# Performance work log

Measured on AMD Instinct MI355X. Metric: run time of the kernel, lower is better.

## Reference

```python
import jax, jax.numpy as jnp
import numpy as np

N = 100000   # nodes
C = 128      # in_channels
K = 32       # n_super_nodes
B = 64       # graphs (num segments)


def setup_inputs() -> dict:
    key = jax.random.key(0)
    k_x, k_b, k_w1, k_b1, k_w2, k_b2 = jax.random.split(key, 6)
    x = jax.random.normal(k_x, (N, C), dtype=jnp.float32)
    batch = jnp.sort(jax.random.randint(k_b, (N,), 0, B))
    # assign_mlp params: Linear(C,C) -> ReLU -> Linear(C,K); stored as [in,out]
    W1 = jax.random.normal(k_w1, (C, C), dtype=jnp.float32) / np.sqrt(C)
    b1 = jax.random.normal(k_b1, (C,), dtype=jnp.float32) * 0.01
    W2 = jax.random.normal(k_w2, (C, K), dtype=jnp.float32) / np.sqrt(C)
    b2 = jax.random.normal(k_b2, (K,), dtype=jnp.float32) * 0.01
    return {"x": x, "batch": batch, "W1": W1, "b1": b1, "W2": W2, "b2": b2}


def reference(x, batch, W1, b1, W2, b2):
    # assignment logits: MLP over node features
    h = jax.nn.relu(x @ W1 + b1)          # [N, C]
    s = jax.nn.softmax(h @ W2 + b2, axis=-1)  # [N, K]
    # outer product per node, then scatter-sum by graph id
    x_expanded = x[:, None, :] * s[:, :, None]  # [N, K, C]
    out = jax.ops.segment_sum(x_expanded, batch, num_segments=B)  # [B, K, C]
    return (out, s)
```

## Files before the change

### kernel.cpp

```cpp
#include <hip/hip_runtime.h>
#include <hip/hip_bf16.h>

#define NN 100000
#define CC 128
#define KK 32
#define BB 64
#define PS 16

typedef __bf16 bf16x8 __attribute__((ext_vector_type(8)));
typedef float  f32x4  __attribute__((ext_vector_type(4)));

__device__ __forceinline__ unsigned short f2bf(float v) {
    union { float f; unsigned u; } a; a.f = v;
    unsigned r = a.u + 0x7FFF + ((a.u >> 16) & 1);
    return (unsigned short)(r >> 16);
}
__device__ __forceinline__ float bf2f(unsigned short h) {
    union { unsigned u; float f; } a; a.u = ((unsigned)h) << 16;
    return a.f;
}
__device__ __forceinline__ void unpack_hilo(uint4 a, uint4 b,
                                            bf16x8& hi8, bf16x8& lo8) {
    union { uint4 v[2]; unsigned short s[16]; } U;
    U.v[0] = a; U.v[1] = b;
    union { unsigned short s[8]; bf16x8 v; } H, L;
    #pragma unroll
    for (int j = 0; j < 8; ++j) { H.s[j] = U.s[2 * j]; L.s[j] = U.s[2 * j + 1]; }
    hi8 = H.v; lo8 = L.v;
}

__global__ __launch_bounds__(256) void hp_prep(const int* __restrict__ batch,
                                               const float* __restrict__ W1,
                                               const float* __restrict__ W2,
                                               int* __restrict__ bounds,
                                               unsigned short* __restrict__ w1f,
                                               unsigned short* __restrict__ w2f) {
    if (blockIdx.x == 0 && threadIdx.x <= BB) {
        const int b = threadIdx.x;
        int lo = 0, hi = NN;
        while (lo < hi) {
            const int mid = (lo + hi) >> 1;
            if (batch[mid] < b) lo = mid + 1; else hi = mid;
        }
        bounds[b] = lo;
    }
    const int t = blockIdx.x * 256 + threadIdx.x;
    for (int idx = t; idx < 16384; idx += 2048) {
        const int j    = idx & 7;
        const int lane = (idx >> 3) & 63;
        const int nt   = (idx >> 9) & 7;
        const int kt   = idx >> 12;
        const int k = kt * 32 + (lane >> 4) * 8 + j;
        const int n = nt * 16 + (lane & 15);
        const float w = W1[k * CC + n];
        const unsigned short h = f2bf(w);
        w1f[idx]         = h;
        w1f[16384 + idx] = f2bf(w - bf2f(h));
    }
    for (int idx = t; idx < 4096; idx += 2048) {
        const int j    = idx & 7;
        const int lane = (idx >> 3) & 63;
        const int nt   = (idx >> 9) & 1;
        const int kt   = idx >> 10;
        const int k = kt * 32 + (lane >> 4) * 8 + j;
        const int n = nt * 16 + (lane & 15);
        const float w = W2[k * KK + n];
        const unsigned short h = f2bf(w);
        w2f[idx]        = h;
        w2f[4096 + idx] = f2bf(w - bf2f(h));
    }
}

__global__ __launch_bounds__(256, 6) void hp_mlp(
    const float* __restrict__ x,
    const unsigned short* __restrict__ w1f,
    const unsigned short* __restrict__ w2f,
    const float* __restrict__ b1,
    const float* __restrict__ b2,
    float* __restrict__ s_out,
    unsigned short* __restrict__ xb,
    unsigned short* __restrict__ sb)
{
    __shared__ __align__(16) char uni[16896];
    __shared__ float lgT[32][36];
    __shared__ float redm[4][32];
    __shared__ float reds[4][32];

    unsigned short* xa   = (unsigned short*)uni;
    unsigned int*   hs16 = (unsigned int*)uni;

    const int t    = threadIdx.x;
    const int wave = __builtin_amdgcn_readfirstlane(t >> 6);
    const int lane = t & 63;
    const int base = blockIdx.x * 32;

    #pragma unroll
    for (int mt = 0; mt < 2; ++mt) {
        const int q  = mt * 4 + wave;
        const int n  = base + mt * 16 + (lane & 15);
        const int ck = wave * 32 + (lane >> 4) * 8;
        const float4 va = *(const float4*)(x + (size_t)n * CC + ck);
        const float4 vb = *(const float4*)(x + (size_t)n * CC + ck + 4);
        const float v[8] = {va.x, va.y, va.z, va.w, vb.x, vb.y, vb.z, vb.w};
        unsigned short hi[8], lo[8];
        #pragma unroll
        for (int j = 0; j < 8; ++j) {
            hi[j] = f2bf(v[j]);
            lo[j] = f2bf(v[j] - bf2f(hi[j]));
        }
        unsigned short* d0 = xa + (q * 64 + lane) * 8;
        unsigned short* d1 = d0 + 4096;
        *(ushort4*)(d0)     = make_ushort4(hi[0], hi[1], hi[2], hi[3]);
        *(ushort4*)(d0 + 4) = make_ushort4(hi[4], hi[5], hi[6], hi[7]);
        *(ushort4*)(d1)     = make_ushort4(lo[0], lo[1], lo[2], lo[3]);
        *(ushort4*)(d1 + 4) = make_ushort4(lo[4], lo[5], lo[6], lo[7]);
    }

    #pragma unroll
    for (int cc = 0; cc < 2; ++cc) {
        const int ct = wave * 2 + cc;
        const int c  = ct * 16 + (lane & 15);
        const int nb = base + (lane >> 4) * 8;
        unsigned short hb[8];
        #pragma unroll
        for (int j = 0; j < 8; ++j)
            hb[j] = f2bf(x[(size_t)(nb + j) * CC + c]);
        unsigned short* dp = xb + ((size_t)(blockIdx.x * 8 + ct) * 64 + lane) * 8;
        *(ushort4*)(dp)     = make_ushort4(hb[0], hb[1], hb[2], hb[3]);
        *(ushort4*)(dp + 4) = make_ushort4(hb[4], hb[5], hb[6], hb[7]);
    }
    __syncthreads();

    f32x4 acc[2][2];
    #pragma unroll
    for (int mt = 0; mt < 2; ++mt)
        #pragma unroll
        for (int nl = 0; nl < 2; ++nl)
            acc[mt][nl] = (f32x4){0.f, 0.f, 0.f, 0.f};

    #pragma unroll
    for (int kt = 0; kt < 4; ++kt) {
        bf16x8 ah[2], al[2];
        #pragma unroll
        for (int mt = 0; mt < 2; ++mt) {
            ah[mt] = *(const bf16x8*)(xa + ((mt * 4 + kt) * 64 + lane) * 8);
            al[mt] = *(const bf16x8*)(xa + 4096 + ((mt * 4 + kt) * 64 + lane) * 8);
        }
        #pragma unroll
        for (int nl = 0; nl < 2; ++nl) {
            const int nt = 2 * wave + nl;
            const bf16x8 wh = *(const bf16x8*)(w1f + ((kt * 8 + nt) * 64 + lane) * 8);
            const bf16x8 wl = *(const bf16x8*)(w1f + 16384 + ((kt * 8 + nt) * 64 + lane) * 8);
            #pragma unroll
            for (int mt = 0; mt < 2; ++mt) {
                acc[mt][nl] = __builtin_amdgcn_mfma_f32_16x16x32_bf16(ah[mt], wh, acc[mt][nl], 0, 0, 0);
                acc[mt][nl] = __builtin_amdgcn_mfma_f32_16x16x32_bf16(al[mt], wh, acc[mt][nl], 0, 0, 0);
                acc[mt][nl] = __builtin_amdgcn_mfma_f32_16x16x32_bf16(ah[mt], wl, acc[mt][nl], 0, 0, 0);
            }
        }
    }
    __syncthreads();

    #pragma unroll
    for (int nl = 0; nl < 2; ++nl) {
        const int c = (2 * wave + nl) * 16 + (lane & 15);
        const float bv = b1[c];
        #pragma unroll
        for (int mt = 0; mt < 2; ++mt)
            #pragma unroll
            for (int r = 0; r < 4; ++r) {
                const int node = mt * 16 + (lane >> 4) * 4 + r;
                const float h = fmaxf(acc[mt][nl][r] + bv, 0.f);
                const unsigned short hi = f2bf(h);
                const unsigned short lo = f2bf(h - bf2f(hi));
                hs16[node * 132 + c] = (unsigned)hi | ((unsigned)lo << 16);
            }
    }
    __syncthreads();

    {
        const int mt2 = wave & 1, nt2 = wave >> 1;
        f32x4 dacc = (f32x4){0.f, 0.f, 0.f, 0.f};
        #pragma unroll
        for (int kt = 0; kt < 4; ++kt) {
            const unsigned* hp = hs16 + (mt2 * 16 + (lane & 15)) * 132
                                      + kt * 32 + (lane >> 4) * 8;
            const uint4 u0 = *(const uint4*)hp;
            const uint4 u1 = *(const uint4*)(hp + 4);
            bf16x8 ah, al;
            unpack_hilo(u0, u1, ah, al);
            const bf16x8 wh = *(const bf16x8*)(w2f + ((kt * 2 + nt2) * 64 + lane) * 8);
            const bf16x8 wl = *(const bf16x8*)(w2f + 4096 + ((kt * 2 + nt2) * 64 + lane) * 8);
            dacc = __builtin_amdgcn_mfma_f32_16x16x32_bf16(ah, wh, dacc, 0, 0, 0);
            dacc = __builtin_amdgcn_mfma_f32_16x16x32_bf16(al, wh, dacc, 0, 0, 0);
            dacc = __builtin_amdgcn_mfma_f32_16x16x32_bf16(ah, wl, dacc, 0, 0, 0);
        }
        const int kcol = nt2 * 16 + (lane & 15);
        #pragma unroll
        for (int r = 0; r < 4; ++r) {
            const int node = mt2 * 16 + (lane >> 4) * 4 + r;
            lgT[node][kcol] = dacc[r];
        }
    }
    __syncthreads();

    const int node = lane & 31;
    const int koff = ((lane >> 5) << 4) + wave * 4;
    const float4 bv2 = *(const float4*)(b2 + koff);
    const float4 lv  = *(const float4*)&lgT[node][koff];
    float lg[4] = {lv.x + bv2.x, lv.y + bv2.y, lv.z + bv2.z, lv.w + bv2.w};

    float m = fmaxf(fmaxf(lg[0], lg[1]), fmaxf(lg[2], lg[3]));
    m = fmaxf(m, __shfl_xor(m, 32));
    if (lane < 32) redm[wave][lane] = m;
    __syncthreads();
    const float M = fmaxf(fmaxf(redm[0][node], redm[1][node]),
                          fmaxf(redm[2][node], redm[3][node]));
    const float e0 = __expf(lg[0] - M);
    const float e1 = __expf(lg[1] - M);
    const float e2 = __expf(lg[2] - M);
    const float e3 = __expf(lg[3] - M);
    float sp = (e0 + e1) + (e2 + e3);
    sp += __shfl_xor(sp, 32);
    if (lane < 32) reds[wave][lane] = sp;
    __syncthreads();
    const float S = (reds[0][node] + reds[1][node]) + (reds[2][node] + reds[3][node]);
    const float inv = 1.f / S;
    const float4 s4 = make_float4(e0 * inv, e1 * inv, e2 * inv, e3 * inv);
    *(float4*)(s_out + (size_t)(base + node) * KK + koff) = s4;
    *(float4*)&lgT[node][koff] = s4;
    __syncthreads();

    if (wave < 2) {
        const int k  = wave * 16 + (lane & 15);
        const int r0 = (lane >> 4) * 8;
        unsigned short v[8];
        #pragma unroll
        for (int j = 0; j < 8; ++j)
            v[j] = f2bf(lgT[r0 + j][k]);
        unsigned short* dp = sb + ((size_t)(blockIdx.x * 2 + wave) * 64 + lane) * 8;
        *(ushort4*)(dp)     = make_ushort4(v[0], v[1], v[2], v[3]);
        *(ushort4*)(dp + 4) = make_ushort4(v[4], v[5], v[6], v[7]);
    }
}

__global__ __launch_bounds__(256) void hp_pool(
    const unsigned short* __restrict__ xb,
    const unsigned short* __restrict__ sb,
    const int* __restrict__ bounds,
    float* __restrict__ part)
{
    const int b = blockIdx.x / PS;
    const int p = blockIdx.x - b * PS;
    const int wave = __builtin_amdgcn_readfirstlane(threadIdx.x >> 6);
    const int lane = threadIdx.x & 63;

    const int gs = bounds[b], ge = bounds[b + 1];
    const int c0g = gs >> 5;
    const int cnt = ((ge + 31) >> 5) - c0g;
    const int ch0 = c0g + (cnt * p) / PS;
    const int ch1 = c0g + (cnt * (p + 1)) / PS;

    const int mt    = wave & 1;
    const int chalf = wave >> 1;
    const int nrow  = (lane >> 4) * 8;

    f32x4 acc[4];
    #pragma unroll
    for (int i = 0; i < 4; ++i) acc[i] = (f32x4){0.f, 0.f, 0.f, 0.f};

    for (int ch = ch0; ch < ch1; ++ch) {
        union { ushort4 u[2]; unsigned short s[8]; bf16x8 v; } A;
        const unsigned short* ap = sb + ((size_t)(ch * 2 + mt) * 64 + lane) * 8;
        A.u[0] = *(const ushort4*)ap;
        A.u[1] = *(const ushort4*)(ap + 4);
        const int nb = ch * 32 + nrow;
        #pragma unroll
        for (int j = 0; j < 8; ++j)
            if (nb + j < gs || nb + j >= ge) A.s[j] = 0;
        #pragma unroll
        for (int i = 0; i < 4; ++i) {
            const int ct = chalf * 4 + i;
            const bf16x8 Bv = *(const bf16x8*)(xb + ((size_t)(ch * 8 + ct) * 64 + lane) * 8);
            acc[i] = __builtin_amdgcn_mfma_f32_16x16x32_bf16(A.v, Bv, acc[i], 0, 0, 0);
        }
    }

    float* op = part + (size_t)blockIdx.x * KK * CC;
    #pragma unroll
    for (int i = 0; i < 4; ++i) {
        const int c = (chalf * 4 + i) * 16 + (lane & 15);
        #pragma unroll
        for (int r = 0; r < 4; ++r) {
            const int k = mt * 16 + (lane >> 4) * 4 + r;
            op[k * CC + c] = acc[i][r];
        }
    }
}

__global__ __launch_bounds__(256) void hp_reduce(const float* __restrict__ part,
                                                 float* __restrict__ out) {
    const int i = (blockIdx.x * 256 + threadIdx.x) * 4;
    if (i < BB * KK * CC) {
        const int b = i >> 12;
        const int j = i & 4095;
        const float* pp = part + (size_t)b * PS * 4096 + j;
        float4 r = make_float4(0.f, 0.f, 0.f, 0.f);
        #pragma unroll 4
        for (int q = 0; q < PS; ++q) {
            const float4 v = *(const float4*)(pp + (size_t)q * 4096);
            r.x += v.x; r.y += v.y; r.z += v.z; r.w += v.w;
        }
        *(float4*)(out + i) = r;
    }
}

extern "C" void kernel_launch(void* const* d_in, const int* in_sizes, int n_in,
                              void* d_out, int out_size, void* d_ws, size_t ws_size,
                              hipStream_t stream) {
    const float* x     = (const float*)d_in[0];
    const int*   batch = (const int*)d_in[1];
    const float* W1    = (const float*)d_in[2];
    const float* b1    = (const float*)d_in[3];
    const float* W2    = (const float*)d_in[4];
    const float* b2    = (const float*)d_in[5];

    float* out = (float*)d_out;
    float* s   = out + (size_t)BB * KK * CC;

    char* ws = (char*)d_ws;
    int*            bounds = (int*)ws;
    unsigned short* w1f    = (unsigned short*)(ws + 1024);
    unsigned short* w2f    = (unsigned short*)(ws + 66560);
    unsigned short* xb     = (unsigned short*)(ws + 82944);
    unsigned short* sb     = (unsigned short*)(ws + 82944 + 25600000);
    float*          part   = (float*)(ws + 82944 + 25600000 + 6400000);

    hp_prep<<<8, 256, 0, stream>>>(batch, W1, W2, bounds, w1f, w2f);
    hp_mlp<<<NN / 32, 256, 0, stream>>>(x, w1f, w2f, b1, b2, s, xb, sb);
    hp_pool<<<BB * PS, 256, 0, stream>>>(xb, sb, bounds, part);
    hp_reduce<<<BB * KK * CC / (256 * 4), 256, 0, stream>>>(part, out);
}
```

Before: 133.4 us.

## Replace partial-sum reduce kernel with float atomics and fold output zeroing into prep

Removes the hp_reduce launch and the partial buffer. hp_pool now adds its per-split results straight into the output with hardware float atomics, and hp_prep (grown to 64 blocks) zeroes the output and does the weight conversion without loops. The change also switches bf16 conversion to the native cast, uses v_perm for hi/lo unpacking, and widens stores to uint4. The aim is to save one kernel launch and the round trip of partial sums through memory, in exchange for atomic contention (16 writers per element) and a nondeterministic summation order.

Result: slower. 139.1 us (+4.3%).

```diff
diff --git a/kernel.cpp b/kernel.cpp
--- a/kernel.cpp
+++ b/kernel.cpp
@@ -11,9 +11,9 @@
 typedef float  f32x4  __attribute__((ext_vector_type(4)));
 
 __device__ __forceinline__ unsigned short f2bf(float v) {
-    union { float f; unsigned u; } a; a.f = v;
-    unsigned r = a.u + 0x7FFF + ((a.u >> 16) & 1);
-    return (unsigned short)(r >> 16);
+    union { __bf16 h; unsigned short s; } u;
+    u.h = (__bf16)v;
+    return u.s;
 }
 __device__ __forceinline__ float bf2f(unsigned short h) {
     union { unsigned u; float f; } a; a.u = ((unsigned)h) << 16;
@@ -21,12 +21,24 @@
 }
 __device__ __forceinline__ void unpack_hilo(uint4 a, uint4 b,
                                             bf16x8& hi8, bf16x8& lo8) {
-    union { uint4 v[2]; unsigned short s[16]; } U;
-    U.v[0] = a; U.v[1] = b;
-    union { unsigned short s[8]; bf16x8 v; } H, L;
-    #pragma unroll
-    for (int j = 0; j < 8; ++j) { H.s[j] = U.s[2 * j]; L.s[j] = U.s[2 * j + 1]; }
+    union { unsigned u[4]; bf16x8 v; } H, L;
+    H.u[0] = __builtin_amdgcn_perm(a.y, a.x, 0x05040100u);
+    H.u[1] = __builtin_amdgcn_perm(a.w, a.z, 0x05040100u);
+    H.u[2] = __builtin_amdgcn_perm(b.y, b.x, 0x05040100u);
+    H.u[3] = __builtin_amdgcn_perm(b.w, b.z, 0x05040100u);
+    L.u[0] = __builtin_amdgcn_perm(a.y, a.x, 0x07060302u);
+    L.u[1] = __builtin_amdgcn_perm(a.w, a.z, 0x07060302u);
+    L.u[2] = __builtin_amdgcn_perm(b.y, b.x, 0x07060302u);
+    L.u[3] = __builtin_amdgcn_perm(b.w, b.z, 0x07060302u);
     hi8 = H.v; lo8 = L.v;
+}
+
+__device__ __forceinline__ void atomAddF(float* p, float v) {
+#if defined(__gfx950__) || defined(__gfx942__) || defined(__gfx90a__)
+    unsafeAtomicAdd(p, v);
+#else
+    atomicAdd(p, v);
+#endif
 }
 
 __global__ __launch_bounds__(256) void hp_prep(const int* __restrict__ batch,
@@ -34,7 +46,8 @@
                                                const float* __restrict__ W2,
                                                int* __restrict__ bounds,
                                                unsigned short* __restrict__ w1f,
-                                               unsigned short* __restrict__ w2f) {
+                                               unsigned short* __restrict__ w2f,
+                                               float* __restrict__ out_zero) {
     if (blockIdx.x == 0 && threadIdx.x <= BB) {
         const int b = threadIdx.x;
         int lo = 0, hi = NN;
@@ -45,7 +58,8 @@
         bounds[b] = lo;
     }
     const int t = blockIdx.x * 256 + threadIdx.x;
-    for (int idx = t; idx < 16384; idx += 2048) {
+    {
+        const int idx  = t;
         const int j    = idx & 7;
         const int lane = (idx >> 3) & 63;
         const int nt   = (idx >> 9) & 7;
@@ -57,7 +71,8 @@
         w1f[idx]         = h;
         w1f[16384 + idx] = f2bf(w - bf2f(h));
     }
-    for (int idx = t; idx < 4096; idx += 2048) {
+    if (t < 4096) {
+        const int idx  = t;
         const int j    = idx & 7;
         const int lane = (idx >> 3) & 63;
         const int nt   = (idx >> 9) & 1;
@@ -69,6 +84,10 @@
         w2f[idx]        = h;
         w2f[4096 + idx] = f2bf(w - bf2f(h));
     }
+    const float4 z = make_float4(0.f, 0.f, 0.f, 0.f);
+    #pragma unroll
+    for (int i = t; i < BB * KK * CC / 4; i += 16384)
+        *(float4*)(out_zero + (size_t)i * 4) = z;
 }
 
 __global__ __launch_bounds__(256, 6) void hp_mlp(
@@ -102,18 +121,15 @@
         const float4 va = *(const float4*)(x + (size_t)n * CC + ck);
         const float4 vb = *(const float4*)(x + (size_t)n * CC + ck + 4);
         const float v[8] = {va.x, va.y, va.z, va.w, vb.x, vb.y, vb.z, vb.w};
-        unsigned short hi[8], lo[8];
+        union { unsigned short s[8]; uint4 u; } H, L;
         #pragma unroll
         for (int j = 0; j < 8; ++j) {
-            hi[j] = f2bf(v[j]);
-            lo[j] = f2bf(v[j] - bf2f(hi[j]));
+            H.s[j] = f2bf(v[j]);
+            L.s[j] = f2bf(v[j] - bf2f(H.s[j]));
         }
         unsigned short* d0 = xa + (q * 64 + lane) * 8;
-        unsigned short* d1 = d0 + 4096;
-        *(ushort4*)(d0)     = make_ushort4(hi[0], hi[1], hi[2], hi[3]);
-        *(ushort4*)(d0 + 4) = make_ushort4(hi[4], hi[5], hi[6], hi[7]);
-        *(ushort4*)(d1)     = make_ushort4(lo[0], lo[1], lo[2], lo[3]);
-        *(ushort4*)(d1 + 4) = make_ushort4(lo[4], lo[5], lo[6], lo[7]);
+        *(uint4*)(d0)        = H.u;
+        *(uint4*)(d0 + 4096) = L.u;
     }
 
     #pragma unroll
@@ -121,13 +137,12 @@
         const int ct = wave * 2 + cc;
         const int c  = ct * 16 + (lane & 15);
         const int nb = base + (lane >> 4) * 8;
-        unsigned short hb[8];
+        union { unsigned short s[8]; uint4 u; } Hb;
         #pragma unroll
         for (int j = 0; j < 8; ++j)
-            hb[j] = f2bf(x[(size_t)(nb + j) * CC + c]);
+            Hb.s[j] = f2bf(x[(size_t)(nb + j) * CC + c]);
         unsigned short* dp = xb + ((size_t)(blockIdx.x * 8 + ct) * 64 + lane) * 8;
-        *(ushort4*)(dp)     = make_ushort4(hb[0], hb[1], hb[2], hb[3]);
-        *(ushort4*)(dp + 4) = make_ushort4(hb[4], hb[5], hb[6], hb[7]);
+        *(uint4*)dp = Hb.u;
     }
     __syncthreads();
 
@@ -234,13 +249,12 @@
     if (wave < 2) {
         const int k  = wave * 16 + (lane & 15);
         const int r0 = (lane >> 4) * 8;
-        unsigned short v[8];
+        union { unsigned short s[8]; uint4 u; } V;
         #pragma unroll
         for (int j = 0; j < 8; ++j)
-            v[j] = f2bf(lgT[r0 + j][k]);
+            V.s[j] = f2bf(lgT[r0 + j][k]);
         unsigned short* dp = sb + ((size_t)(blockIdx.x * 2 + wave) * 64 + lane) * 8;
-        *(ushort4*)(dp)     = make_ushort4(v[0], v[1], v[2], v[3]);
-        *(ushort4*)(dp + 4) = make_ushort4(v[4], v[5], v[6], v[7]);
+        *(uint4*)dp = V.u;
     }
 }
 
@@ -248,7 +262,7 @@
     const unsigned short* __restrict__ xb,
     const unsigned short* __restrict__ sb,
     const int* __restrict__ bounds,
-    float* __restrict__ part)
+    float* __restrict__ out)
 {
     const int b = blockIdx.x / PS;
     const int p = blockIdx.x - b * PS;
@@ -270,10 +284,8 @@
     for (int i = 0; i < 4; ++i) acc[i] = (f32x4){0.f, 0.f, 0.f, 0.f};
 
     for (int ch = ch0; ch < ch1; ++ch) {
-        union { ushort4 u[2]; unsigned short s[8]; bf16x8 v; } A;
-        const unsigned short* ap = sb + ((size_t)(ch * 2 + mt) * 64 + lane) * 8;
-        A.u[0] = *(const ushort4*)ap;
-        A.u[1] = *(const ushort4*)(ap + 4);
+        union { uint4 u; unsigned short s[8]; bf16x8 v; } A;
+        A.u = *(const uint4*)(sb + ((size_t)(ch * 2 + mt) * 64 + lane) * 8);
         const int nb = ch * 32 + nrow;
         #pragma unroll
         for (int j = 0; j < 8; ++j)
@@ -286,32 +298,15 @@
         }
     }
 
-    float* op = part + (size_t)blockIdx.x * KK * CC;
+    float* op = out + (size_t)b * KK * CC;
     #pragma unroll
     for (int i = 0; i < 4; ++i) {
         const int c = (chalf * 4 + i) * 16 + (lane & 15);
         #pragma unroll
         for (int r = 0; r < 4; ++r) {
             const int k = mt * 16 + (lane >> 4) * 4 + r;
-            op[k * CC + c] = acc[i][r];
-        }
-    }
-}
-
-__global__ __launch_bounds__(256) void hp_reduce(const float* __restrict__ part,
-                                                 float* __restrict__ out) {
-    const int i = (blockIdx.x * 256 + threadIdx.x) * 4;
-    if (i < BB * KK * CC) {
-        const int b = i >> 12;
-        const int j = i & 4095;
-        const float* pp = part + (size_t)b * PS * 4096 + j;
-        float4 r = make_float4(0.f, 0.f, 0.f, 0.f);
-        #pragma unroll 4
-        for (int q = 0; q < PS; ++q) {
-            const float4 v = *(const float4*)(pp + (size_t)q * 4096);
-            r.x += v.x; r.y += v.y; r.z += v.z; r.w += v.w;
-        }
-        *(float4*)(out + i) = r;
+            atomAddF(op + k * CC + c, acc[i][r]);
+        }
     }
 }
 
@@ -334,10 +329,8 @@
     unsigned short* w2f    = (unsigned short*)(ws + 66560);
     unsigned short* xb     = (unsigned short*)(ws + 82944);
     unsigned short* sb     = (unsigned short*)(ws + 82944 + 25600000);
-    float*          part   = (float*)(ws + 82944 + 25600000 + 6400000);
-
-    hp_prep<<<8, 256, 0, stream>>>(batch, W1, W2, bounds, w1f, w2f);
+
+    hp_prep<<<64, 256, 0, stream>>>(batch, W1, W2, bounds, w1f, w2f, out);
     hp_mlp<<<NN / 32, 256, 0, stream>>>(x, w1f, w2f, b1, b2, s, xb, sb);
-    hp_pool<<<BB * PS, 256, 0, stream>>>(xb, sb, bounds, part);
-    hp_reduce<<<BB * KK * CC / (256 * 4), 256, 0, stream>>>(part, out);
-}
+    hp_pool<<<BB * PS, 256, 0, stream>>>(xb, sb, bounds, out);
+}
```
